# Kernel tuning notes

Hardware: AMD Instinct MI355X
Metric: run time of the kernel (lower is better)

The kernel has to match this reference:

```python
import jax, jax.numpy as jnp
import numpy as np

N_DRUG = 572
D = 512
K = 64          # neighbor_sample_size
T = 30000       # tail entities
R = 200         # relations
MAX_DEG = 32    # padded invariant_adj neighbor count
EPS = 1e-5


def setup_inputs() -> dict:
    key = jax.random.key(0)
    ks = jax.random.split(key, 10)
    return {
        "drug_embed_W": jax.random.normal(ks[0], (N_DRUG, D), jnp.float32),
        "rela_embed_W": jax.random.normal(ks[1], (R, D), jnp.float32),
        "ent_embed_W": jax.random.normal(ks[2], (T, D), jnp.float32),
        "Wa": jax.random.normal(ks[3], (D, D), jnp.float32) / np.float32(np.sqrt(D)),
        "lin_W": jax.random.normal(ks[4], (2 * D, D), jnp.float32) / np.float32(np.sqrt(2 * D)),
        "lin_b": jnp.zeros((D,), jnp.float32),
        "gamma": jnp.ones((D,), jnp.float32),
        "beta": jnp.zeros((D,), jnp.float32),
        "drug_name": jnp.arange(N_DRUG, dtype=jnp.int64 if jax.config.jax_enable_x64 else jnp.int32),
        "adj_tail": jax.random.randint(ks[5], (N_DRUG, K), 0, T),
        "adj_relation": jax.random.randint(ks[6], (N_DRUG, K), 0, R),
        "nbr_idx": jax.random.randint(ks[7], (N_DRUG, MAX_DEG), 0, N_DRUG),
        "nbr_deg": jax.random.randint(ks[8], (N_DRUG,), 0, MAX_DEG),
        "epoch": 2,
    }


def _forward(drug_embed_W, rela_embed_W, ent_embed_W, Wa, lin_W, lin_b, gamma, beta,
             drug_name, adj_tail, adj_relation, nbr_idx, nbr_deg, epoch):
    drug_e = drug_embed_W[drug_name]          # [N, D]
    rela = rela_embed_W[adj_relation]         # [N, K, D]
    ent = ent_embed_W[adj_tail]               # [N, K, D]

    # relation-aware attention over sampled neighbors (AttentionLayer)
    q = drug_e @ Wa                           # [N, D]
    scores = jnp.einsum('nd,nkd->nk', q, rela) * (1.0 / np.float32(np.sqrt(D)))
    attn = jax.nn.softmax(scores, axis=1)     # [N, K]
    agg = jnp.einsum('nk,nkd->nd', attn, ent) # [N, D]

    # Linear1: Linear(2D->D) + ReLU + BatchNorm1d (training-mode batch stats)
    h = jnp.concatenate([agg, drug_e], axis=1) @ lin_W + lin_b
    h = jax.nn.relu(h)
    mean = jnp.mean(h, axis=0)
    var = jnp.var(h, axis=0)                  # biased, as torch BN normalization
    drug_f = (h - mean) * jax.lax.rsqrt(var + EPS) * gamma + beta

    if epoch > 1:
        # sequential per-node neighbor-mean smoothing (in-place semantics)
        mask = (jnp.arange(MAX_DEG)[None, :] < nbr_deg[:, None])  # [N, MAX_DEG]

        def step(f, i):
            pos = nbr_idx[i]
            m = mask[i][:, None].astype(f.dtype)
            s = jnp.sum(f[pos] * m, axis=0)
            deg = nbr_deg[i]
            avg = s / jnp.maximum(deg, 1).astype(f.dtype)
            new = jnp.where(deg > 0, (avg + f[i]) * 0.5, f[i])
            return f.at[i].set(new), None

        drug_f, _ = jax.lax.scan(step, drug_f, jnp.arange(N_DRUG))
    return drug_f


def reference(drug_embed_W, rela_embed_W, ent_embed_W, Wa, lin_W, lin_b, gamma, beta,
              drug_name, adj_tail, adj_relation, nbr_idx, nbr_deg, epoch):
    return _forward(drug_embed_W, rela_embed_W, ent_embed_W, Wa, lin_W, lin_b, gamma, beta,
                    drug_name, adj_tail, adj_relation, nbr_idx, nbr_deg, epoch)
```

## Files before the change

kernel.cpp:

```cpp
#include <hip/hip_runtime.h>

#define N_DRUG 572
#define DIM 512
#define MAXDEG 32
#define FS 17

__global__ __launch_bounds__(256) void prep_kernel(
    const float* __restrict__ Wa, const float* __restrict__ relaW,
    const float* __restrict__ linW, float* __restrict__ linP,
    float* __restrict__ relaP)
{
    const int b = blockIdx.x;
    const int t = threadIdx.x;
    if (b < 512) {
        const int g = b * 256 + t;
        const int c = g & 511, k4 = g >> 9;
        const float4 v = make_float4(linW[(size_t)(k4 * 4 + 0) * 512 + c],
                                     linW[(size_t)(k4 * 4 + 1) * 512 + c],
                                     linW[(size_t)(k4 * 4 + 2) * 512 + c],
                                     linW[(size_t)(k4 * 4 + 3) * 512 + c]);
        *(float4*)&linP[((size_t)(c >> 6) * 256 + k4) * 256 + (c & 63) * 4] = v;
        return;
    }
    const int bb = b - 512;
    const int rb = bb >> 5, kb = bb & 31;
    const int wv = t >> 6, l = t & 63;
    const int r0 = rb * 16 + wv * 4;
    const int k0 = kb * 16;

    float a[4][8];
    #pragma unroll
    for (int rr = 0; rr < 4; ++rr) {
        const float4* ap = (const float4*)(relaW + (size_t)min(r0 + rr, 199) * 512 + l * 8);
        const float4 x = ap[0], y = ap[1];
        a[rr][0] = x.x; a[rr][1] = x.y; a[rr][2] = x.z; a[rr][3] = x.w;
        a[rr][4] = y.x; a[rr][5] = y.y; a[rr][6] = y.z; a[rr][7] = y.w;
    }
    float acc[64];
    #pragma unroll
    for (int i = 0; i < 64; ++i) acc[i] = 0.f;
    #pragma unroll
    for (int kk = 0; kk < 16; ++kk) {
        const float4* bp = (const float4*)(Wa + (size_t)(k0 + kk) * 512 + l * 8);
        const float4 x = bp[0], y = bp[1];
        const float bv[8] = {x.x, x.y, x.z, x.w, y.x, y.y, y.z, y.w};
        #pragma unroll
        for (int rr = 0; rr < 4; ++rr) {
            float s = acc[rr * 16 + kk];
            #pragma unroll
            for (int j = 0; j < 8; ++j) s = fmaf(a[rr][j], bv[j], s);
            acc[rr * 16 + kk] = s;
        }
    }
    #pragma unroll
    for (int off = 1; off <= 32; off <<= 1) {
        #pragma unroll
        for (int i = 0; i < 64; ++i) acc[i] += __shfl_xor(acc[i], off, 64);
    }
    float outv = acc[0];
    #pragma unroll
    for (int i = 1; i < 64; ++i) outv = (l == i) ? acc[i] : outv;
    const int rr = l >> 4, kk = l & 15;
    if (r0 + rr < 200) relaP[(size_t)(r0 + rr) * 512 + k0 + kk] = outv;
}

__global__ __launch_bounds__(256) void attn_kernel(
    const float* __restrict__ drugW, const float* __restrict__ relaP,
    const float* __restrict__ entW, const int* __restrict__ dn,
    const int* __restrict__ adj_tail, const int* __restrict__ adj_rel,
    float* __restrict__ cat)
{
    __shared__ float at[64];
    __shared__ int tails[64];
    __shared__ int rels[64];
    const int d = blockIdx.x;
    const int t = threadIdx.x;
    const int w = t >> 6, lane = t & 63;

    if (t < 64) {
        tails[t] = adj_tail[d * 64 + t];
        rels[t]  = adj_rel[d * 64 + t];
    }
    const int rd = dn[d];
    float qv[8];
    {
        const float4* qp = (const float4*)(drugW + (size_t)rd * 512 + lane * 8);
        const float4 x = qp[0], y = qp[1];
        qv[0] = x.x; qv[1] = x.y; qv[2] = x.z; qv[3] = x.w;
        qv[4] = y.x; qv[5] = y.y; qv[6] = y.z; qv[7] = y.w;
    }
    __syncthreads();

    #pragma unroll 4
    for (int kk = 0; kk < 16; ++kk) {
        const int k = w * 16 + kk;
        const float4* p = (const float4*)(relaP + (size_t)rels[k] * 512 + lane * 8);
        const float4 x = p[0], y = p[1];
        float s = 0.f;
        s = fmaf(qv[0], x.x, s); s = fmaf(qv[1], x.y, s);
        s = fmaf(qv[2], x.z, s); s = fmaf(qv[3], x.w, s);
        s = fmaf(qv[4], y.x, s); s = fmaf(qv[5], y.y, s);
        s = fmaf(qv[6], y.z, s); s = fmaf(qv[7], y.w, s);
        #pragma unroll
        for (int off = 32; off >= 1; off >>= 1) s += __shfl_xor(s, off, 64);
        if (lane == 0) at[k] = s * 0.0441941738241592f;
    }
    __syncthreads();

    if (w == 0) {
        const float s = at[lane];
        float m = s;
        #pragma unroll
        for (int off = 32; off >= 1; off >>= 1) m = fmaxf(m, __shfl_xor(m, off, 64));
        const float e = __expf(s - m);
        float sum = e;
        #pragma unroll
        for (int off = 32; off >= 1; off >>= 1) sum += __shfl_xor(sum, off, 64);
        at[lane] = e / sum;
    }
    __syncthreads();

    {
        const int c2 = t * 2;
        float a0 = 0.f, a1 = 0.f;
        #pragma unroll 8
        for (int k = 0; k < 64; ++k) {
            const float ak = at[k];
            const float2 e = *(const float2*)(entW + (size_t)tails[k] * 512 + c2);
            a0 = fmaf(ak, e.x, a0);
            a1 = fmaf(ak, e.y, a1);
        }
        float* o = cat + (size_t)d * 1024;
        *(float2*)&o[c2] = make_float2(a0, a1);
        const float2 de = *(const float2*)(drugW + (size_t)rd * 512 + c2);
        *(float2*)&o[512 + c2] = de;
    }
}

__global__ __launch_bounds__(256) void gemm_h(
    const float* __restrict__ A, const float* __restrict__ linP,
    const float* __restrict__ bias, float* __restrict__ out)
{
    __shared__ float red[4][8][64];
    const int t = threadIdx.x;
    const int wv = t >> 6, lane = t & 63;
    const int r0 = blockIdx.x * 8;

    const float* wp = linP + ((size_t)blockIdx.y * 256 + wv * 64) * 256 + lane * 4;
    const float* ap[8];
    #pragma unroll
    for (int r = 0; r < 8; ++r)
        ap[r] = A + (size_t)min(r0 + r, N_DRUG - 1) * 1024 + wv * 256;

    float acc[8] = {0.f, 0.f, 0.f, 0.f, 0.f, 0.f, 0.f, 0.f};
    #pragma unroll 4
    for (int k4 = 0; k4 < 64; ++k4) {
        const float4 w = *(const float4*)(wp + (size_t)k4 * 256);
        #pragma unroll
        for (int r = 0; r < 8; ++r) {
            const float4 a = *(const float4*)(ap[r] + k4 * 4);
            acc[r] = fmaf(a.x, w.x, acc[r]);
            acc[r] = fmaf(a.y, w.y, acc[r]);
            acc[r] = fmaf(a.z, w.z, acc[r]);
            acc[r] = fmaf(a.w, w.w, acc[r]);
        }
    }
    #pragma unroll
    for (int r = 0; r < 8; ++r) red[wv][r][lane] = acc[r];
    __syncthreads();

    #pragma unroll
    for (int u = 0; u < 2; ++u) {
        const int o = u * 256 + t;
        const int r = o >> 6, cc = o & 63;
        if (r0 + r < N_DRUG) {
            const float v = red[0][r][cc] + red[1][r][cc] + red[2][r][cc] + red[3][r][cc]
                          + bias[blockIdx.y * 64 + cc];
            out[(size_t)(r0 + r) * 512 + blockIdx.y * 64 + cc] = fmaxf(v, 0.f);
        }
    }
}

__global__ __launch_bounds__(512) void scan_kernel(
    float* hout, const float* __restrict__ gamma, const float* __restrict__ beta,
    const int* __restrict__ nbr_idx, const int* __restrict__ nbr_deg,
    const int* __restrict__ epoch)
{
    __shared__ float fs[(N_DRUG + 1) * FS];
    __shared__ alignas(16) unsigned short offs[N_DRUG * MAXDEG];
    __shared__ float2 ivw[N_DRUG];
    __shared__ int   mxs[N_DRUG];
    __shared__ float part[2][32][16];
    __shared__ float bnp[2][16];
    __shared__ int   genext[2];
    __shared__ int   ge0s;

    const int t  = threadIdx.x;
    const int c  = t & 15;
    const int h  = (t >> 4) & 1;
    const int j  = t >> 5;
    const int rr = t >> 4;
    const int c0 = blockIdx.x * 16;

    for (int i = t; i < N_DRUG; i += 512) {
        const int d = nbr_deg[i];
        ivw[i] = (d > 0) ? make_float2(0.5f / (float)d, 0.5f) : make_float2(0.f, 1.f);
        const int4* np = (const int4*)&nbr_idx[i * MAXDEG];
        unsigned* op = (unsigned*)&offs[i * MAXDEG];
        int mx = -1;
        #pragma unroll
        for (int u = 0; u < 8; ++u) {
            int4 qq = np[u];
            const int b = u * 4;
            qq.x = (b + 0 < d) ? qq.x : N_DRUG;
            qq.y = (b + 1 < d) ? qq.y : N_DRUG;
            qq.z = (b + 2 < d) ? qq.z : N_DRUG;
            qq.w = (b + 3 < d) ? qq.w : N_DRUG;
            mx = max(mx, (qq.x < i) ? qq.x : -1);
            mx = max(mx, (qq.y < i) ? qq.y : -1);
            mx = max(mx, (qq.z < i) ? qq.z : -1);
            mx = max(mx, (qq.w < i) ? qq.w : -1);
            op[2 * u]     = (unsigned)(qq.x * FS) | ((unsigned)(qq.y * FS) << 16);
            op[2 * u + 1] = (unsigned)(qq.z * FS) | ((unsigned)(qq.w * FS) << 16);
        }
        mxs[i] = mx;
    }

    {
        float sl = 0.f, ql = 0.f;
        for (int r = rr; r < N_DRUG; r += 32) {
            const float v = hout[(size_t)r * DIM + c0 + c];
            fs[r * FS + c] = v;
            sl += v;
            ql = fmaf(v, v, ql);
        }
        part[0][rr][c] = sl;
        part[1][rr][c] = ql;
    }
    if (t < FS) fs[N_DRUG * FS + t] = 0.f;
    __syncthreads();

    if (t < 16) {
        float s = 0.f, sq = 0.f;
        #pragma unroll
        for (int k = 0; k < 32; ++k) { s += part[0][k][t]; sq += part[1][k][t]; }
        const float mean = s * (1.f / N_DRUG);
        const float var = sq * (1.f / N_DRUG) - mean * mean;
        const float rstd = rsqrtf(var + 1e-5f);
        const float scl = gamma[c0 + t] * rstd;
        bnp[0][t] = scl;
        bnp[1][t] = beta[c0 + t] - mean * scl;
    }
    if ((t >> 6) == 7) {
        const int l = t & 63;
        const int jj = 1 + l;
        const bool flag = (l >= 15) || (jj >= N_DRUG) || (mxs[min(jj, N_DRUG - 1)] >= 0);
        const unsigned long long b = __ballot(flag) & 0xFFFFULL;
        if (l == 0) ge0s = 1 + (int)__builtin_ctzll(b);
    }
    __syncthreads();

    {
        const float scl = bnp[0][c];
        const float shf = bnp[1][c];
        for (int r = rr; r < N_DRUG; r += 32)
            fs[r * FS + c] = fmaf(fs[r * FS + c], scl, shf);
    }
    __syncthreads();

    if (epoch[0] > 1) {
        int gs = 0, ge = ge0s;
        uint4 ca, cb;
        {
            const uint4* p = (const uint4*)&offs[min(j, N_DRUG - 1) * MAXDEG + h * 16];
            ca = p[0]; cb = p[1];
        }
        int par = 0;
        while (gs < N_DRUG) {
            const bool pred = (gs + j) < ge;
            float s0 = 0.f, s1 = 0.f;
#define G2(W) { s0 += fs[(W & 0xffffu) + c]; s1 += fs[(W >> 16) + c]; }
            if (pred) { G2(ca.x) G2(ca.y) G2(ca.z) G2(ca.w)
                        G2(cb.x) G2(cb.y) G2(cb.z) G2(cb.w) }
#undef G2
            uint4 na, nb;
            {
                const uint4* p = (const uint4*)&offs[min(ge + j, N_DRUG - 1) * MAXDEG + h * 16];
                na = p[0]; nb = p[1];
            }
            float nv = 0.f;
            if (pred) {
                const float cur = fs[(gs + j) * FS + c];
                const float2 iw = ivw[gs + j];
                float sh = s0 + s1;
                sh += __shfl_xor(sh, 16, 64);
                nv = fmaf(sh, iw.x, cur * iw.y);
            }
            if ((t >> 6) == 7) {
                const int l = t & 63;
                const int jj = ge + 1 + l;
                const bool flag = (l >= 15) || (jj >= N_DRUG) ||
                                  (mxs[min(jj, N_DRUG - 1)] >= ge);
                const unsigned long long b = __ballot(flag) & 0xFFFFULL;
                if (l == 0) genext[par] = ge + 1 + (int)__builtin_ctzll(b);
            }
            __syncthreads();
            if (pred && h == 0) fs[(gs + j) * FS + c] = nv;
            __syncthreads();
            gs = ge;
            ge = genext[par];
            par ^= 1;
            ca = na; cb = nb;
        }
    }
    __syncthreads();

    for (int r = rr; r < N_DRUG; r += 32)
        hout[(size_t)r * DIM + c0 + c] = fs[r * FS + c];
}

extern "C" void kernel_launch(void* const* d_in, const int* in_sizes, int n_in,
                              void* d_out, int out_size, void* d_ws, size_t ws_size,
                              hipStream_t stream)
{
    const float* drugW = (const float*)d_in[0];
    const float* relaW = (const float*)d_in[1];
    const float* entW  = (const float*)d_in[2];
    const float* Wa    = (const float*)d_in[3];
    const float* linW  = (const float*)d_in[4];
    const float* linb  = (const float*)d_in[5];
    const float* gamma = (const float*)d_in[6];
    const float* beta  = (const float*)d_in[7];
    const int* drug_name = (const int*)d_in[8];
    const int* adj_tail  = (const int*)d_in[9];
    const int* adj_rel   = (const int*)d_in[10];
    const int* nbr_idx   = (const int*)d_in[11];
    const int* nbr_deg   = (const int*)d_in[12];
    const int* epoch     = (const int*)d_in[13];

    float* out = (float*)d_out;

    float* linP  = (float*)d_ws;
    float* relaP = (float*)((char*)d_ws + 2097152);
    float* cat   = (float*)((char*)d_ws + 2506752);

    prep_kernel<<<928, 256, 0, stream>>>(Wa, relaW, linW, linP, relaP);
    attn_kernel<<<N_DRUG, 256, 0, stream>>>(drugW, relaP, entW, drug_name,
                                            adj_tail, adj_rel, cat);
    gemm_h<<<dim3(72, 8), 256, 0, stream>>>(cat, linP, linb, out);
    scan_kernel<<<32, 512, 0, stream>>>(out, gamma, beta, nbr_idx, nbr_deg, epoch);
}
```

Measured before the change: 238.9 us.

## Widen gemm_h tiles to 128 columns with 8-wave split-K and 2 outputs per lane

Reshapes the Linear1 GEMM so each block covers 128 output columns with 512 threads. The 8 waves each take 128 of the K dimension, and each lane computes two columns per row. This reuses every A load across two weight columns, halves the grid's y dimension, and makes each block read the A rows half as many times in total. The cost is a larger shared-memory reduction across 8 waves and fewer blocks, which reduces parallelism for a kernel that is small relative to the sequential scan.

```diff
diff --git a/kernel.cpp b/kernel.cpp
--- a/kernel.cpp
+++ b/kernel.cpp
@@ -137,46 +137,58 @@
     }
 }
 
-__global__ __launch_bounds__(256) void gemm_h(
+__global__ __launch_bounds__(512) void gemm_h(
     const float* __restrict__ A, const float* __restrict__ linP,
     const float* __restrict__ bias, float* __restrict__ out)
 {
-    __shared__ float red[4][8][64];
+    __shared__ float red[8][8][128];
     const int t = threadIdx.x;
     const int wv = t >> 6, lane = t & 63;
     const int r0 = blockIdx.x * 8;
-
-    const float* wp = linP + ((size_t)blockIdx.y * 256 + wv * 64) * 256 + lane * 4;
+    const int half = lane >> 5;
+    const int cw = (lane * 2) & 63;
+
+    const float* wp = linP + ((size_t)(blockIdx.y * 2 + half) * 256 + wv * 32) * 256
+                    + cw * 4;
     const float* ap[8];
     #pragma unroll
     for (int r = 0; r < 8; ++r)
-        ap[r] = A + (size_t)min(r0 + r, N_DRUG - 1) * 1024 + wv * 256;
-
-    float acc[8] = {0.f, 0.f, 0.f, 0.f, 0.f, 0.f, 0.f, 0.f};
-    #pragma unroll 4
-    for (int k4 = 0; k4 < 64; ++k4) {
-        const float4 w = *(const float4*)(wp + (size_t)k4 * 256);
+        ap[r] = A + (size_t)min(r0 + r, N_DRUG - 1) * 1024 + wv * 128;
+
+    float acc0[8] = {0.f, 0.f, 0.f, 0.f, 0.f, 0.f, 0.f, 0.f};
+    float acc1[8] = {0.f, 0.f, 0.f, 0.f, 0.f, 0.f, 0.f, 0.f};
+    #pragma unroll 2
+    for (int k4 = 0; k4 < 32; ++k4) {
+        const float4 w0 = *(const float4*)(wp + (size_t)k4 * 256);
+        const float4 w1 = *(const float4*)(wp + (size_t)k4 * 256 + 4);
         #pragma unroll
         for (int r = 0; r < 8; ++r) {
             const float4 a = *(const float4*)(ap[r] + k4 * 4);
-            acc[r] = fmaf(a.x, w.x, acc[r]);
-            acc[r] = fmaf(a.y, w.y, acc[r]);
-            acc[r] = fmaf(a.z, w.z, acc[r]);
-            acc[r] = fmaf(a.w, w.w, acc[r]);
-        }
-    }
-    #pragma unroll
-    for (int r = 0; r < 8; ++r) red[wv][r][lane] = acc[r];
+            acc0[r] = fmaf(a.x, w0.x, acc0[r]);
+            acc0[r] = fmaf(a.y, w0.y, acc0[r]);
+            acc0[r] = fmaf(a.z, w0.z, acc0[r]);
+            acc0[r] = fmaf(a.w, w0.w, acc0[r]);
+            acc1[r] = fmaf(a.x, w1.x, acc1[r]);
+            acc1[r] = fmaf(a.y, w1.y, acc1[r]);
+            acc1[r] = fmaf(a.z, w1.z, acc1[r]);
+            acc1[r] = fmaf(a.w, w1.w, acc1[r]);
+        }
+    }
+    #pragma unroll
+    for (int r = 0; r < 8; ++r)
+        *(float2*)&red[wv][r][lane * 2] = make_float2(acc0[r], acc1[r]);
     __syncthreads();
 
     #pragma unroll
     for (int u = 0; u < 2; ++u) {
-        const int o = u * 256 + t;
-        const int r = o >> 6, cc = o & 63;
+        const int o = u * 512 + t;
+        const int r = o >> 7, cc = o & 127;
         if (r0 + r < N_DRUG) {
-            const float v = red[0][r][cc] + red[1][r][cc] + red[2][r][cc] + red[3][r][cc]
-                          + bias[blockIdx.y * 64 + cc];
-            out[(size_t)(r0 + r) * 512 + blockIdx.y * 64 + cc] = fmaxf(v, 0.f);
+            float v = red[0][r][cc];
+            #pragma unroll
+            for (int w = 1; w < 8; ++w) v += red[w][r][cc];
+            v += bias[blockIdx.y * 128 + cc];
+            out[(size_t)(r0 + r) * 512 + blockIdx.y * 128 + cc] = fmaxf(v, 0.f);
         }
     }
 }
@@ -347,6 +359,6 @@
     prep_kernel<<<928, 256, 0, stream>>>(Wa, relaW, linW, linP, relaP);
     attn_kernel<<<N_DRUG, 256, 0, stream>>>(drugW, relaP, entW, drug_name,
                                             adj_tail, adj_rel, cat);
-    gemm_h<<<dim3(72, 8), 256, 0, stream>>>(cat, linP, linb, out);
+    gemm_h<<<dim3(72, 4), 512, 0, stream>>>(cat, linP, linb, out);
     scan_kernel<<<32, 512, 0, stream>>>(out, gamma, beta, nbr_idx, nbr_deg, epoch);
 }
```

Result: faster. 227.1 us (-4.9%).
